# Kernel tuning notes

Hardware: AMD Instinct MI355X
Metric: run time of the kernel (lower is better)

Reference implementation:

```python
import jax, jax.numpy as jnp
import numpy as np

D_MODEL = 128; D_STATE = 64; HEADDIM = 32; D_CONV = 4; EXPAND = 2
D_INNER = EXPAND * D_MODEL          # 256
NHEADS = D_INNER // HEADDIM         # 8
NGROUPS = 1
D_CONV_CH = D_INNER + 2 * NGROUPS * D_STATE      # 384
D_IN_PROJ = 2 * D_INNER + 2 * NGROUPS * D_STATE + NHEADS  # 648


def _mamba2(u, Win, convw, convb, dtb, Alog, Dp, normw, Wout):
    # u: (B, L, d_model). Mamba2 forward (ngroups=1, rmsnorm gated, no in/out bias).
    B, L, _ = u.shape
    zxbcdt = u @ Win                                   # (B,L,648)
    z, xBC, dt = jnp.split(zxbcdt, [D_INNER, D_INNER + D_CONV_CH], axis=-1)
    # depthwise causal conv1d (kernel D_CONV) + SiLU
    xp = jnp.pad(xBC, ((0, 0), (D_CONV - 1, 0), (0, 0)))
    xconv = sum(xp[:, k:k + L, :] * convw[k] for k in range(D_CONV)) + convb
    xBC = jax.nn.silu(xconv)
    x, Bm, Cm = jnp.split(xBC, [D_INNER, D_INNER + NGROUPS * D_STATE], axis=-1)
    dt = jax.nn.softplus(dt + dtb)                     # (B,L,H)
    A = -jnp.exp(Alog)                                 # (H,)
    xh = x.reshape(B, L, NHEADS, HEADDIM)              # (B,L,H,P)
    dA = jnp.exp(dt * A)                               # (B,L,H)

    def step(h, inp):
        dA_t, dt_t, B_t, C_t, x_t = inp
        h = h * dA_t[:, :, None, None] + jnp.einsum('bh,bn,bhp->bhpn', dt_t, B_t, x_t)
        y = jnp.einsum('bhpn,bn->bhp', h, C_t)
        return h, y

    h0 = jnp.zeros((B, NHEADS, HEADDIM, D_STATE), dtype=u.dtype)
    xs = (jnp.moveaxis(dA, 1, 0), jnp.moveaxis(dt, 1, 0), jnp.moveaxis(Bm, 1, 0),
          jnp.moveaxis(Cm, 1, 0), jnp.moveaxis(xh, 1, 0))
    _, ys = jax.lax.scan(step, h0, xs)
    y = jnp.moveaxis(ys, 0, 1) + Dp[None, None, :, None] * xh   # skip D
    y = y.reshape(B, L, D_INNER)
    # RMSNormGated (norm_before_gate=False): rmsnorm(y * silu(z)) * weight
    y = y * jax.nn.silu(z)
    y = y * jax.lax.rsqrt(jnp.mean(y * y, axis=-1, keepdims=True) + 1e-5) * normw
    return y @ Wout


def _cross_attn(x, ctx, Wq, bq, Wk, bk, Wv, bv, Wo, bo):
    Q = x @ Wq + bq
    K = ctx @ Wk + bk
    V = ctx @ Wv + bv
    att = jax.nn.softmax(jnp.einsum('bqd,bkd->bqk', Q, K) * (D_MODEL ** -0.5), axis=-1)
    return jnp.einsum('bqk,bkd->bqd', att, V) @ Wo + bo


def setup_inputs() -> dict:
    key = jax.random.key(0)
    ks = jax.random.split(key, 8)
    B, L = 2048, 8

    def lin(k, fi, fo):
        return jax.random.normal(k, (fi, fo), jnp.float32) / np.sqrt(fi)

    def mamba_params(kseq):
        k = jax.random.split(kseq, 6)
        dt = jax.random.uniform(k[3], (NHEADS,), minval=0.001, maxval=0.1)
        return {
            'Win': lin(k[0], D_MODEL, D_IN_PROJ),
            'convw': jax.random.normal(k[1], (D_CONV, D_CONV_CH), jnp.float32) * 0.2,
            'convb': jnp.zeros((D_CONV_CH,), jnp.float32),
            'dtb': dt + jnp.log(-jnp.expm1(-dt)),  # inverse softplus
            'Alog': jnp.log(jax.random.uniform(k[4], (NHEADS,), minval=1.0, maxval=16.0)),
            'D': jnp.ones((NHEADS,), jnp.float32),
            'normw': jnp.ones((D_INNER,), jnp.float32),
            'Wout': lin(k[5], D_INNER, D_MODEL),
        }

    inp = {
        'st_feature': jax.random.normal(ks[0], (B, L, D_MODEL), jnp.float32),
        'exp_feature': jax.random.normal(ks[1], (B, L, D_MODEL), jnp.float32),
    }
    for pref, p in (('st_', mamba_params(ks[2])), ('ex_', mamba_params(ks[3]))):
        for n, v in p.items():
            inp[pref + n] = v

    def ca(kseq, pref):
        k = jax.random.split(kseq, 4)
        d = {}
        for n, kk in zip(('Wq', 'Wk', 'Wv', 'Wo'), k):
            d[pref + n] = lin(kk, D_MODEL, D_MODEL)
            d[pref + 'b' + n[1]] = jnp.zeros((D_MODEL,), jnp.float32)
        return d

    inp.update(ca(ks[4], 'cx_'))  # cross_atten_exp
    inp.update(ca(ks[5], 'cs_'))  # cross_atten_st
    inp['mlp_W'] = lin(ks[6], 8 * 2 * D_MODEL, 1024)
    inp['mlp_b'] = jnp.zeros((1024,), jnp.float32)
    return inp


def reference(st_feature, exp_feature,
              st_Win, st_convw, st_convb, st_dtb, st_Alog, st_D, st_normw, st_Wout,
              ex_Win, ex_convw, ex_convb, ex_dtb, ex_Alog, ex_D, ex_normw, ex_Wout,
              cx_Wq, cx_bq, cx_Wk, cx_bk, cx_Wv, cx_bv, cx_Wo, cx_bo,
              cs_Wq, cs_bq, cs_Wk, cs_bk, cs_Wv, cs_bv, cs_Wo, cs_bo,
              mlp_W, mlp_b):
    exp_f = _mamba2(exp_feature, ex_Win, ex_convw, ex_convb, ex_dtb, ex_Alog, ex_D, ex_normw, ex_Wout)
    st_f = _mamba2(st_feature, st_Win, st_convw, st_convb, st_dtb, st_Alog, st_D, st_normw, st_Wout)
    exp_a = _cross_attn(exp_f, st_f, cx_Wq, cx_bq, cx_Wk, cx_bk, cx_Wv, cx_bv, cx_Wo, cx_bo)
    st_a = _cross_attn(st_f, exp_f, cs_Wq, cs_bq, cs_Wk, cs_bk, cs_Wv, cs_bv, cs_Wo, cs_bo)
    x = jnp.concatenate([st_a, exp_a], axis=-1)        # (B, 8, 256)
    x = x.reshape(x.shape[0], -1)                      # (B, 2048)
    return x @ mlp_W + mlp_b
```

## Files before the change

kernel.cpp:

```cpp
#include <hip/hip_runtime.h>
#include <hip/hip_bf16.h>
#include <math.h>

#define B_SZ 2048
#define L_SEQ 8
#define DMODEL 128
#define DSTATE 64
#define HEADDIM 32
#define DCONV 4
#define DINNER 256
#define NHEADS 8
#define DCONVCH 384
#define DINPROJ 648
#define NPAD 656

typedef short bf16x8 __attribute__((ext_vector_type(8)));
typedef float floatx4 __attribute__((ext_vector_type(4)));

__device__ __forceinline__ float siluf(float x) {
    return x / (1.f + expf(-x));
}
__device__ __forceinline__ float bf2f(unsigned short h) {
    unsigned int u = ((unsigned int)h) << 16;
    return __builtin_bit_cast(float, u);
}
__device__ __forceinline__ unsigned short f2bf(float f) {
    __hip_bfloat16 b = __float2bfloat16(f);
    return __builtin_bit_cast(unsigned short, b);
}
__device__ __forceinline__ void unpack8(bf16x8 v, float* o) {
    #pragma unroll
    for (int j = 0; j < 8; ++j) o[j] = bf2f((unsigned short)v[j]);
}

__global__ __launch_bounds__(256) void prep_weights(
    const float* __restrict__ st_Win, const float* __restrict__ ex_Win,
    const float* __restrict__ st_Wout, const float* __restrict__ ex_Wout,
    const float* __restrict__ cs_Wq, const float* __restrict__ cs_Wk,
    const float* __restrict__ cs_Wv, const float* __restrict__ cs_Wo,
    const float* __restrict__ cx_Wq, const float* __restrict__ cx_Wk,
    const float* __restrict__ cx_Wv, const float* __restrict__ cx_Wo,
    unsigned short* __restrict__ winT_st, unsigned short* __restrict__ winT_ex,
    unsigned short* __restrict__ woutT_st, unsigned short* __restrict__ woutT_ex,
    unsigned short* __restrict__ attnWT)
{
    int blk = blockIdx.x;
    if (blk < 656) {
        const float* src = blk < 328 ? st_Win : ex_Win;
        unsigned short* dst = blk < 328 ? winT_st : winT_ex;
        int idx = (blk % 328) * 256 + threadIdx.x;
        if (idx >= NPAD * 128) return;
        int n = idx / 128, k = idx % 128;
        float v = (n < DINPROJ) ? src[k * DINPROJ + n] : 0.f;
        dst[idx] = f2bf(v);
    } else if (blk < 912) {
        const float* src = blk < 784 ? st_Wout : ex_Wout;
        unsigned short* dst = blk < 784 ? woutT_st : woutT_ex;
        int idx = ((blk - 656) % 128) * 256 + threadIdx.x;
        int n = idx / 256, k = idx % 256;
        dst[idx] = f2bf(src[k * 128 + n]);
    } else {
        int b2 = blk - 912;
        int mat = b2 >> 6;
        const float* src = mat == 0 ? cs_Wq : mat == 1 ? cs_Wk : mat == 2 ? cs_Wv :
                           mat == 3 ? cs_Wo : mat == 4 ? cx_Wq : mat == 5 ? cx_Wk :
                           mat == 6 ? cx_Wv : cx_Wo;
        int e = (b2 & 63) * 256 + threadIdx.x;
        int n = e >> 7, k = e & 127;
        attnWT[mat * 16384 + n * 128 + k] = f2bf(src[k * 128 + n]);
    }
}

#define LDK 136
#define LDZ 648
#define LDY 264
__global__ __launch_bounds__(256, 4) void mamba_dual(
    const float* __restrict__ u_ex, const float* __restrict__ u_st,
    const unsigned short* __restrict__ WinT_ex, const unsigned short* __restrict__ WinT_st,
    const float* __restrict__ convw_ex, const float* __restrict__ convw_st,
    const float* __restrict__ convb_ex, const float* __restrict__ convb_st,
    const float* __restrict__ dtb_ex, const float* __restrict__ dtb_st,
    const float* __restrict__ Alog_ex, const float* __restrict__ Alog_st,
    const float* __restrict__ Dp_ex, const float* __restrict__ Dp_st,
    const float* __restrict__ normw_ex, const float* __restrict__ normw_st,
    const unsigned short* __restrict__ WoutT_ex, const unsigned short* __restrict__ WoutT_st,
    unsigned short* __restrict__ out_ex, unsigned short* __restrict__ out_st)
{
    const int which = blockIdx.x >> 10;
    const float* u = which ? u_st : u_ex;
    const unsigned short* WinT = which ? WinT_st : WinT_ex;
    const float* convw = which ? convw_st : convw_ex;
    const float* convb = which ? convb_st : convb_ex;
    const float* dtb = which ? dtb_st : dtb_ex;
    const float* Alog = which ? Alog_st : Alog_ex;
    const float* Dp = which ? Dp_st : Dp_ex;
    const float* normw = which ? normw_st : normw_ex;
    const unsigned short* WoutT = which ? WoutT_st : WoutT_ex;
    unsigned short* outf = which ? out_st : out_ex;

    const int tid = threadIdx.x;
    const int lane = tid & 63;
    const int wave = tid >> 6;
    const int l15 = lane & 15;
    const int q8 = (lane >> 4) * 8;
    const int row0 = (lane >> 4) * 4;
    const int grow0 = (blockIdx.x & 1023) * 16;

    __shared__ __align__(16) unsigned short uA[16 * LDK];
    __shared__ __align__(16) unsigned short zx[16 * LDZ];
    __shared__ __align__(16) unsigned short yb[16 * LDY];
    __shared__ float dtraw[16][8];
    __shared__ float dtv[2][8][8];
    __shared__ float cum[2][8][8];
    __shared__ float Gm[2][8][8];
    __shared__ float red[16][32];
    __shared__ float rstd[16];
    float* coefp = (float*)uA;

    for (int i = tid; i < 512; i += 256) {
        int r = i >> 5, k4 = (i & 31) * 4;
        float4 v = *(const float4*)(u + (size_t)(grow0 + r) * DMODEL + k4);
        ushort4 h;
        h.x = f2bf(v.x); h.y = f2bf(v.y); h.z = f2bf(v.z); h.w = f2bf(v.w);
        *(ushort4*)(uA + r * LDK + k4) = h;
    }
    __syncthreads();

    {
        bf16x8 af[4];
        #pragma unroll
        for (int kk = 0; kk < 4; ++kk)
            af[kk] = *(const bf16x8*)(uA + l15 * LDK + kk * 32 + q8);
        for (int nt = wave; nt < 41; nt += 4) {
            floatx4 acc = {0.f, 0.f, 0.f, 0.f};
            const unsigned short* bp = WinT + (size_t)(nt * 16 + l15) * 128 + q8;
            #pragma unroll
            for (int kk = 0; kk < 4; ++kk) {
                bf16x8 bf = *(const bf16x8*)(bp + kk * 32);
                acc = __builtin_amdgcn_mfma_f32_16x16x32_bf16(af[kk], bf, acc, 0, 0, 0);
            }
            if (nt == 40) {
                if (l15 < 8) {
                    #pragma unroll
                    for (int r = 0; r < 4; ++r)
                        dtraw[row0 + r][l15] = acc[r];
                }
            } else {
                #pragma unroll
                for (int r = 0; r < 4; ++r)
                    zx[(row0 + r) * LDZ + nt * 16 + l15] = f2bf(acc[r]);
            }
        }
    }
    __syncthreads();

    float cv[3][8];
    {
        #pragma unroll
        for (int it = 0; it < 3; ++it) {
            int i = tid + it * 256;
            int r = i / 48, g = i % 48;
            int c0 = g * 8;
            int l = r & 7, bloc = r >> 3;
            float s[8];
            float4 cb0 = *(const float4*)(convb + c0);
            float4 cb1 = *(const float4*)(convb + c0 + 4);
            s[0] = cb0.x; s[1] = cb0.y; s[2] = cb0.z; s[3] = cb0.w;
            s[4] = cb1.x; s[5] = cb1.y; s[6] = cb1.z; s[7] = cb1.w;
            #pragma unroll
            for (int k = 0; k < DCONV; ++k) {
                int lp = l + k - (DCONV - 1);
                if (lp >= 0) {
                    bf16x8 v = *(const bf16x8*)(zx + (bloc * 8 + lp) * LDZ + 256 + c0);
                    float vf[8];
                    unpack8(v, vf);
                    float4 w0 = *(const float4*)(convw + k * DCONVCH + c0);
                    float4 w1 = *(const float4*)(convw + k * DCONVCH + c0 + 4);
                    s[0] += vf[0] * w0.x; s[1] += vf[1] * w0.y;
                    s[2] += vf[2] * w0.z; s[3] += vf[3] * w0.w;
                    s[4] += vf[4] * w1.x; s[5] += vf[5] * w1.y;
                    s[6] += vf[6] * w1.z; s[7] += vf[7] * w1.w;
                }
            }
            #pragma unroll
            for (int j = 0; j < 8; ++j) cv[it][j] = siluf(s[j]);
        }
        if (tid < 128) {
            int r = tid >> 3, h = tid & 7;
            float v = dtraw[r][h] + dtb[h];
            dtv[r >> 3][r & 7][h] = (v > 20.f) ? v : log1pf(expf(v));
        }
    }
    __syncthreads();
    {
        #pragma unroll
        for (int it = 0; it < 3; ++it) {
            int i = tid + it * 256;
            int r = i / 48, c0 = (i % 48) * 8;
            bf16x8 o;
            #pragma unroll
            for (int j = 0; j < 8; ++j) o[j] = (short)f2bf(cv[it][j]);
            *(bf16x8*)(zx + r * LDZ + 256 + c0) = o;
        }
    }
    __syncthreads();

    if (tid < 128) {
        int bloc = tid >> 6, t = (tid >> 3) & 7, s = tid & 7;
        float a = 0.f;
        #pragma unroll
        for (int n = 0; n < DSTATE; n += 8) {
            bf16x8 bv = *(const bf16x8*)(zx + (bloc * 8 + s) * LDZ + 512 + n);
            bf16x8 cvv = *(const bf16x8*)(zx + (bloc * 8 + t) * LDZ + 576 + n);
            float bf_[8], cf_[8];
            unpack8(bv, bf_); unpack8(cvv, cf_);
            #pragma unroll
            for (int j = 0; j < 8; ++j) a += bf_[j] * cf_[j];
        }
        Gm[bloc][t][s] = a;
    } else if (tid < 144) {
        int j = tid - 128;
        int bloc = j >> 3, h = j & 7;
        float c = 0.f;
        for (int l = 0; l < L_SEQ; ++l) { c += dtv[bloc][l][h]; cum[bloc][l][h] = c; }
    }
    __syncthreads();

    for (int i = tid; i < 1024; i += 256) {
        int bloc = i >> 9, t = (i >> 6) & 7, s = (i >> 3) & 7, h = i & 7;
        float A = -expf(Alog[h]);
        coefp[i] = (s <= t)
            ? Gm[bloc][t][s] * expf(A * (cum[bloc][t][h] - cum[bloc][s][h])) * dtv[bloc][s][h]
            : 0.f;
    }
    __syncthreads();

    {
        #pragma unroll
        for (int it = 0; it < 2; ++it) {
            int i = tid + it * 256;
            int r = i >> 5, g = i & 31;
            int c0 = g * 8, h = g >> 2;
            int bloc = r >> 3, t = r & 7;
            float acc[8];
            {
                bf16x8 xv = *(const bf16x8*)(zx + r * LDZ + 256 + c0);
                float xf[8]; unpack8(xv, xf);
                float d = Dp[h];
                #pragma unroll
                for (int j = 0; j < 8; ++j) acc[j] = d * xf[j];
            }
            for (int s = 0; s <= t; ++s) {
                float cf = coefp[((bloc * 8 + t) * 8 + s) * 8 + h];
                bf16x8 xv = *(const bf16x8*)(zx + (bloc * 8 + s) * LDZ + 256 + c0);
                float xf[8]; unpack8(xv, xf);
                #pragma unroll
                for (int j = 0; j < 8; ++j) acc[j] += cf * xf[j];
            }
            bf16x8 zv = *(const bf16x8*)(zx + r * LDZ + c0);
            float zf[8]; unpack8(zv, zf);
            float p = 0.f;
            bf16x8 o;
            #pragma unroll
            for (int j = 0; j < 8; ++j) {
                float y = acc[j] * siluf(zf[j]);
                p += y * y;
                o[j] = (short)f2bf(y);
            }
            *(bf16x8*)(yb + r * LDY + c0) = o;
            red[r][g] = p;
        }
    }
    __syncthreads();
    if (tid < 16) {
        float s = 0.f;
        #pragma unroll
        for (int j = 0; j < 32; ++j) s += red[tid][j];
        rstd[tid] = rsqrtf(s / (float)DINNER + 1e-5f);
    }
    __syncthreads();
    {
        #pragma unroll
        for (int it = 0; it < 2; ++it) {
            int i = tid + it * 256;
            int r = i >> 5, c0 = (i & 31) * 8;
            bf16x8 v = *(const bf16x8*)(yb + r * LDY + c0);
            float vf[8]; unpack8(v, vf);
            float4 w0 = *(const float4*)(normw + c0);
            float4 w1 = *(const float4*)(normw + c0 + 4);
            float rs = rstd[r];
            bf16x8 o;
            o[0] = (short)f2bf(vf[0] * rs * w0.x); o[1] = (short)f2bf(vf[1] * rs * w0.y);
            o[2] = (short)f2bf(vf[2] * rs * w0.z); o[3] = (short)f2bf(vf[3] * rs * w0.w);
            o[4] = (short)f2bf(vf[4] * rs * w1.x); o[5] = (short)f2bf(vf[5] * rs * w1.y);
            o[6] = (short)f2bf(vf[6] * rs * w1.z); o[7] = (short)f2bf(vf[7] * rs * w1.w);
            *(bf16x8*)(yb + r * LDY + c0) = o;
        }
    }
    __syncthreads();

    {
        bf16x8 af[8];
        #pragma unroll
        for (int kk = 0; kk < 8; ++kk)
            af[kk] = *(const bf16x8*)(yb + l15 * LDY + kk * 32 + q8);
        #pragma unroll
        for (int ni = 0; ni < 2; ++ni) {
            int nt = wave * 2 + ni;
            floatx4 acc = {0.f, 0.f, 0.f, 0.f};
            const unsigned short* bp = WoutT + (size_t)(nt * 16 + l15) * 256 + q8;
            #pragma unroll
            for (int kk = 0; kk < 8; ++kk) {
                bf16x8 bf = *(const bf16x8*)(bp + kk * 32);
                acc = __builtin_amdgcn_mfma_f32_16x16x32_bf16(af[kk], bf, acc, 0, 0, 0);
            }
            #pragma unroll
            for (int r = 0; r < 4; ++r)
                outf[(size_t)(grow0 + row0 + r) * DMODEL + nt * 16 + l15] = f2bf(acc[r]);
        }
    }
}

#define ASTR 136
#define VSTR 40
#define PSTR 40
__global__ __launch_bounds__(256) void attn_kernel(
    const unsigned short* __restrict__ st_f,
    const unsigned short* __restrict__ exp_f,
    const unsigned short* __restrict__ WT,
    const float* __restrict__ cs_bq, const float* __restrict__ cs_bk,
    const float* __restrict__ cs_bv, const float* __restrict__ cs_bo,
    const float* __restrict__ cx_bq, const float* __restrict__ cx_bk,
    const float* __restrict__ cx_bv, const float* __restrict__ cx_bo,
    __hip_bfloat16* __restrict__ x)
{
    const int tid = threadIdx.x;
    const int lane = tid & 63, wave = tid >> 6;
    const int l15 = lane & 15;
    const int q8 = (lane >> 4) * 8;
    const int row0 = (lane >> 4) * 4;
    const int grow0 = blockIdx.x * 16;
    const int b0 = blockIdx.x * 2;
    const float scale = 0.08838834764831845f;

    __shared__ __align__(16) unsigned short stf[16 * ASTR];
    __shared__ __align__(16) unsigned short exf[16 * ASTR];
    __shared__ __align__(16) unsigned short Qs[16 * ASTR];
    __shared__ __align__(16) unsigned short Ks[16 * ASTR];
    __shared__ __align__(16) unsigned short Vt[128 * VSTR];
    __shared__ __align__(16) unsigned short P[16 * PSTR];
    __shared__ __align__(16) unsigned short attv[16 * ASTR];
    __shared__ float Ss[16][17];

    {
        int r = tid >> 4, c8 = (tid & 15) * 8;
        *(uint4*)(stf + r * ASTR + c8) = *(const uint4*)(st_f + (size_t)(grow0 + r) * 128 + c8);
        *(uint4*)(exf + r * ASTR + c8) = *(const uint4*)(exp_f + (size_t)(grow0 + r) * 128 + c8);
    }
    {
        int r = tid >> 1, c = 16 + (tid & 1) * 8;
        uint4 z = {0u, 0u, 0u, 0u};
        *(uint4*)(Vt + r * VSTR + c) = z;
    }
    __syncthreads();

    #pragma unroll
    for (int pass = 0; pass < 2; ++pass) {
        const unsigned short* qsrc = pass ? exf : stf;
        const unsigned short* kvsrc = pass ? stf : exf;
        const unsigned short* Wq = WT + (size_t)pass * 4 * 16384;
        const unsigned short* Wk = Wq + 16384;
        const unsigned short* Wv = Wq + 32768;
        const unsigned short* Wo = Wq + 49152;
        const float* bq = pass ? cx_bq : cs_bq;
        const float* bk = pass ? cx_bk : cs_bk;
        const float* bv = pass ? cx_bv : cs_bv;
        const float* bo = pass ? cx_bo : cs_bo;

        bf16x8 aq[4], akv[4];
        #pragma unroll
        for (int kk = 0; kk < 4; ++kk) {
            aq[kk]  = *(const bf16x8*)(qsrc  + l15 * ASTR + kk * 32 + q8);
            akv[kk] = *(const bf16x8*)(kvsrc + l15 * ASTR + kk * 32 + q8);
        }
        #pragma unroll
        for (int ni = 0; ni < 2; ++ni) {
            int nt = wave * 2 + ni;
            int nc = nt * 16 + l15;
            floatx4 accq = {0.f, 0.f, 0.f, 0.f};
            floatx4 acck = {0.f, 0.f, 0.f, 0.f};
            floatx4 accv = {0.f, 0.f, 0.f, 0.f};
            #pragma unroll
            for (int kk = 0; kk < 4; ++kk) {
                bf16x8 wqf = *(const bf16x8*)(Wq + (size_t)nc * 128 + kk * 32 + q8);
                bf16x8 wkf = *(const bf16x8*)(Wk + (size_t)nc * 128 + kk * 32 + q8);
                bf16x8 wvf = *(const bf16x8*)(Wv + (size_t)nc * 128 + kk * 32 + q8);
                accq = __builtin_amdgcn_mfma_f32_16x16x32_bf16(aq[kk],  wqf, accq, 0, 0, 0);
                acck = __builtin_amdgcn_mfma_f32_16x16x32_bf16(akv[kk], wkf, acck, 0, 0, 0);
                accv = __builtin_amdgcn_mfma_f32_16x16x32_bf16(akv[kk], wvf, accv, 0, 0, 0);
            }
            float bqv = bq[nc], bkv = bk[nc], bvv = bv[nc];
            #pragma unroll
            for (int r = 0; r < 4; ++r) {
                Qs[(row0 + r) * ASTR + nc] = f2bf(accq[r] + bqv);
                Ks[(row0 + r) * ASTR + nc] = f2bf(acck[r] + bkv);
                Vt[nc * VSTR + row0 + r]   = f2bf(accv[r] + bvv);
            }
        }
        __syncthreads();

        if (wave == 0) {
            floatx4 s = {0.f, 0.f, 0.f, 0.f};
            #pragma unroll
            for (int kk = 0; kk < 4; ++kk) {
                bf16x8 a = *(const bf16x8*)(Qs + l15 * ASTR + kk * 32 + q8);
                bf16x8 b = *(const bf16x8*)(Ks + l15 * ASTR + kk * 32 + q8);
                s = __builtin_amdgcn_mfma_f32_16x16x32_bf16(a, b, s, 0, 0, 0);
            }
            #pragma unroll
            for (int r = 0; r < 4; ++r) Ss[row0 + r][l15] = s[r];
        }
        __syncthreads();

        if (tid < 16) {
            int r = tid, c0 = (r >> 3) * 8;
            float v[8], mx = -1e30f;
            #pragma unroll
            for (int c = 0; c < 8; ++c) {
                v[c] = Ss[r][c0 + c] * scale;
                mx = fmaxf(mx, v[c]);
            }
            float sum = 0.f;
            #pragma unroll
            for (int c = 0; c < 8; ++c) { v[c] = expf(v[c] - mx); sum += v[c]; }
            float inv = 1.f / sum;
            #pragma unroll
            for (int c = 0; c < 32; ++c) {
                float pv = (c >= c0 && c < c0 + 8) ? v[c - c0] * inv : 0.f;
                P[r * PSTR + c] = f2bf(pv);
            }
        }
        __syncthreads();

        {
            bf16x8 ap = *(const bf16x8*)(P + l15 * PSTR + q8);
            #pragma unroll
            for (int ni = 0; ni < 2; ++ni) {
                int nc = (wave * 2 + ni) * 16 + l15;
                bf16x8 bv_ = *(const bf16x8*)(Vt + nc * VSTR + q8);
                floatx4 o = {0.f, 0.f, 0.f, 0.f};
                o = __builtin_amdgcn_mfma_f32_16x16x32_bf16(ap, bv_, o, 0, 0, 0);
                #pragma unroll
                for (int r = 0; r < 4; ++r)
                    attv[(row0 + r) * ASTR + nc] = f2bf(o[r]);
            }
        }
        __syncthreads();

        {
            bf16x8 ao[4];
            #pragma unroll
            for (int kk = 0; kk < 4; ++kk)
                ao[kk] = *(const bf16x8*)(attv + l15 * ASTR + kk * 32 + q8);
            #pragma unroll
            for (int ni = 0; ni < 2; ++ni) {
                int nc = (wave * 2 + ni) * 16 + l15;
                floatx4 acc = {0.f, 0.f, 0.f, 0.f};
                #pragma unroll
                for (int kk = 0; kk < 4; ++kk) {
                    bf16x8 wof = *(const bf16x8*)(Wo + (size_t)nc * 128 + kk * 32 + q8);
                    acc = __builtin_amdgcn_mfma_f32_16x16x32_bf16(ao[kk], wof, acc, 0, 0, 0);
                }
                float bov = bo[nc];
                #pragma unroll
                for (int r = 0; r < 4; ++r) {
                    int rr = row0 + r;
                    int bb = b0 + (rr >> 3), q = rr & 7;
                    x[(size_t)bb * 2048 + q * 256 + pass * 128 + nc] =
                        __float2bfloat16(acc[r] + bov);
                }
            }
        }
        __syncthreads();
    }
}

__global__ __launch_bounds__(256) void transpose_w_bf16(
    const float* __restrict__ W, unsigned short* __restrict__ Wt)
{
    __shared__ float tile[32][33];
    const int k0 = blockIdx.y * 32;
    const int n0 = blockIdx.x * 32;
    const int tid = threadIdx.x;
    const int c = tid & 31, r0 = tid >> 5;
    for (int rr = r0; rr < 32; rr += 8)
        tile[rr][c] = W[(k0 + rr) * 1024 + n0 + c];
    __syncthreads();
    for (int rr = r0; rr < 32; rr += 8)
        Wt[(size_t)(n0 + rr) * 2048 + k0 + c] = f2bf(tile[c][rr]);
}

#define LDT 40
__global__ __launch_bounds__(256) void mlp_mfma(
    const unsigned short* __restrict__ X,
    const unsigned short* __restrict__ Wt,
    const float* __restrict__ bias,
    float* __restrict__ out)
{
    __shared__ __align__(16) unsigned short As[64 * LDT];
    __shared__ __align__(16) unsigned short Bs[64 * LDT];
    const int tid = threadIdx.x;
    const int wave = tid >> 6, lane = tid & 63;
    const int wm = (wave >> 1) * 32, wn = (wave & 1) * 32;
    const int bm = blockIdx.y * 64, bn = blockIdx.x * 64;

    const int lrow = tid >> 2;
    const int lcol = (tid & 3) * 8;
    const int l15 = lane & 15;
    const int q8 = (lane >> 4) * 8;

    floatx4 acc00 = {0.f, 0.f, 0.f, 0.f};
    floatx4 acc01 = {0.f, 0.f, 0.f, 0.f};
    floatx4 acc10 = {0.f, 0.f, 0.f, 0.f};
    floatx4 acc11 = {0.f, 0.f, 0.f, 0.f};

    const unsigned short* gA = X + (size_t)(bm + lrow) * 2048 + lcol;
    const unsigned short* gB = Wt + (size_t)(bn + lrow) * 2048 + lcol;

    for (int k0 = 0; k0 < 2048; k0 += 32) {
        uint4 av = *(const uint4*)(gA + k0);
        uint4 bv = *(const uint4*)(gB + k0);
        __syncthreads();
        *(uint4*)(As + lrow * LDT + lcol) = av;
        *(uint4*)(Bs + lrow * LDT + lcol) = bv;
        __syncthreads();
        bf16x8 a0 = *(const bf16x8*)(As + (wm + l15) * LDT + q8);
        bf16x8 a1 = *(const bf16x8*)(As + (wm + 16 + l15) * LDT + q8);
        bf16x8 b0 = *(const bf16x8*)(Bs + (wn + l15) * LDT + q8);
        bf16x8 b1 = *(const bf16x8*)(Bs + (wn + 16 + l15) * LDT + q8);
        acc00 = __builtin_amdgcn_mfma_f32_16x16x32_bf16(a0, b0, acc00, 0, 0, 0);
        acc01 = __builtin_amdgcn_mfma_f32_16x16x32_bf16(a0, b1, acc01, 0, 0, 0);
        acc10 = __builtin_amdgcn_mfma_f32_16x16x32_bf16(a1, b0, acc10, 0, 0, 0);
        acc11 = __builtin_amdgcn_mfma_f32_16x16x32_bf16(a1, b1, acc11, 0, 0, 0);
    }

    const int row0 = (lane >> 4) * 4;
    #pragma unroll
    for (int j = 0; j < 2; ++j) {
        int col = bn + wn + j * 16 + l15;
        float bv = bias[col];
        floatx4 aj0 = j ? acc01 : acc00;
        floatx4 aj1 = j ? acc11 : acc10;
        #pragma unroll
        for (int r = 0; r < 4; ++r) {
            out[(size_t)(bm + wm + row0 + r) * 1024 + col] = aj0[r] + bv;
            out[(size_t)(bm + wm + 16 + row0 + r) * 1024 + col] = aj1[r] + bv;
        }
    }
}

extern "C" void kernel_launch(void* const* d_in, const int* in_sizes, int n_in,
                              void* d_out, int out_size, void* d_ws, size_t ws_size,
                              hipStream_t stream) {
    const float* st_feature = (const float*)d_in[0];
    const float* exp_feature = (const float*)d_in[1];
    const float* st_Win = (const float*)d_in[2];
    const float* st_convw = (const float*)d_in[3];
    const float* st_convb = (const float*)d_in[4];
    const float* st_dtb = (const float*)d_in[5];
    const float* st_Alog = (const float*)d_in[6];
    const float* st_D = (const float*)d_in[7];
    const float* st_normw = (const float*)d_in[8];
    const float* st_Wout = (const float*)d_in[9];
    const float* ex_Win = (const float*)d_in[10];
    const float* ex_convw = (const float*)d_in[11];
    const float* ex_convb = (const float*)d_in[12];
    const float* ex_dtb = (const float*)d_in[13];
    const float* ex_Alog = (const float*)d_in[14];
    const float* ex_D = (const float*)d_in[15];
    const float* ex_normw = (const float*)d_in[16];
    const float* ex_Wout = (const float*)d_in[17];
    const float* cx_Wq = (const float*)d_in[18]; const float* cx_bq = (const float*)d_in[19];
    const float* cx_Wk = (const float*)d_in[20]; const float* cx_bk = (const float*)d_in[21];
    const float* cx_Wv = (const float*)d_in[22]; const float* cx_bv = (const float*)d_in[23];
    const float* cx_Wo = (const float*)d_in[24]; const float* cx_bo = (const float*)d_in[25];
    const float* cs_Wq = (const float*)d_in[26]; const float* cs_bq = (const float*)d_in[27];
    const float* cs_Wk = (const float*)d_in[28]; const float* cs_bk = (const float*)d_in[29];
    const float* cs_Wv = (const float*)d_in[30]; const float* cs_bv = (const float*)d_in[31];
    const float* cs_Wo = (const float*)d_in[32]; const float* cs_bo = (const float*)d_in[33];
    const float* mlp_W = (const float*)d_in[34];
    const float* mlp_b = (const float*)d_in[35];

    unsigned short* wsu = (unsigned short*)d_ws;
    unsigned short* st_fb  = wsu;
    unsigned short* exp_fb = st_fb + (size_t)B_SZ * L_SEQ * DMODEL;
    unsigned short* xbuf   = exp_fb + (size_t)B_SZ * L_SEQ * DMODEL;
    unsigned short* wtbuf  = xbuf + (size_t)2048 * 2048;
    unsigned short* winT_st = wtbuf + (size_t)1024 * 2048;
    unsigned short* winT_ex = winT_st + (size_t)NPAD * 128;
    unsigned short* woutT_st = winT_ex + (size_t)NPAD * 128;
    unsigned short* woutT_ex = woutT_st + (size_t)128 * 256;
    unsigned short* attnWT  = woutT_ex + (size_t)128 * 256;

    prep_weights<<<1424, 256, 0, stream>>>(
        st_Win, ex_Win, st_Wout, ex_Wout,
        cs_Wq, cs_Wk, cs_Wv, cs_Wo, cx_Wq, cx_Wk, cx_Wv, cx_Wo,
        winT_st, winT_ex, woutT_st, woutT_ex, attnWT);
    {
        dim3 g(1024 / 32, 2048 / 32);
        transpose_w_bf16<<<g, 256, 0, stream>>>(mlp_W, wtbuf);
    }
    mamba_dual<<<2048, 256, 0, stream>>>(
        exp_feature, st_feature, winT_ex, winT_st,
        ex_convw, st_convw, ex_convb, st_convb,
        ex_dtb, st_dtb, ex_Alog, st_Alog, ex_D, st_D,
        ex_normw, st_normw, woutT_ex, woutT_st,
        exp_fb, st_fb);
    attn_kernel<<<B_SZ / 2, 256, 0, stream>>>(st_fb, exp_fb, attnWT,
                                              cs_bq, cs_bk, cs_bv, cs_bo,
                                              cx_bq, cx_bk, cx_bv, cx_bo,
                                              (__hip_bfloat16*)xbuf);
    {
        dim3 g(1024 / 64, 2048 / 64);
        mlp_mfma<<<g, 256, 0, stream>>>(xbuf, wtbuf, mlp_b, (float*)d_out);
    }
}
```

Baseline: 273.7 us.

## Merge MLP weight transpose into prep, double attention tile, use direct-to-LDS loads in MLP

The MLP weight transpose now runs as extra blocks of the prep_weights launch, which removes one kernel launch. The attention kernel handles 32 rows (4 batches) per block instead of 16, so each projection weight fragment feeds two MFMAs and all four waves share the score computation. The MLP GEMM uses a K-step of 64, XOR-swizzled LDS tiles and global_load_lds direct-to-LDS copies in place of register staging. The cost is more LDS per block and fewer blocks, which can lower occupancy and parallelism in the attention kernel.

```diff
diff --git a/kernel.cpp b/kernel.cpp
--- a/kernel.cpp
+++ b/kernel.cpp
@@ -32,6 +32,11 @@
     #pragma unroll
     for (int j = 0; j < 8; ++j) o[j] = bf2f((unsigned short)v[j]);
 }
+__device__ __forceinline__ void gl_lds16(const unsigned short* g, unsigned short* l) {
+    __builtin_amdgcn_global_load_lds(
+        (const __attribute__((address_space(1))) unsigned int*)g,
+        (__attribute__((address_space(3))) unsigned int*)l, 16, 0, 0);
+}
 
 __global__ __launch_bounds__(256) void prep_weights(
     const float* __restrict__ st_Win, const float* __restrict__ ex_Win,
@@ -40,10 +45,12 @@
     const float* __restrict__ cs_Wv, const float* __restrict__ cs_Wo,
     const float* __restrict__ cx_Wq, const float* __restrict__ cx_Wk,
     const float* __restrict__ cx_Wv, const float* __restrict__ cx_Wo,
+    const float* __restrict__ mlp_W,
     unsigned short* __restrict__ winT_st, unsigned short* __restrict__ winT_ex,
     unsigned short* __restrict__ woutT_st, unsigned short* __restrict__ woutT_ex,
-    unsigned short* __restrict__ attnWT)
+    unsigned short* __restrict__ attnWT, unsigned short* __restrict__ mlpWt)
 {
+    __shared__ float tile[32][33];
     int blk = blockIdx.x;
     if (blk < 656) {
         const float* src = blk < 328 ? st_Win : ex_Win;
@@ -59,7 +66,7 @@
         int idx = ((blk - 656) % 128) * 256 + threadIdx.x;
         int n = idx / 256, k = idx % 256;
         dst[idx] = f2bf(src[k * 128 + n]);
-    } else {
+    } else if (blk < 1424) {
         int b2 = blk - 912;
         int mat = b2 >> 6;
         const float* src = mat == 0 ? cs_Wq : mat == 1 ? cs_Wk : mat == 2 ? cs_Wv :
@@ -68,6 +75,16 @@
         int e = (b2 & 63) * 256 + threadIdx.x;
         int n = e >> 7, k = e & 127;
         attnWT[mat * 16384 + n * 128 + k] = f2bf(src[k * 128 + n]);
+    } else {
+        int b2 = blk - 1424;
+        int n0 = (b2 & 31) * 32, k0 = (b2 >> 5) * 32;
+        const int tid = threadIdx.x;
+        const int c = tid & 31, r0 = tid >> 5;
+        for (int rr = r0; rr < 32; rr += 8)
+            tile[rr][c] = mlp_W[(size_t)(k0 + rr) * 1024 + n0 + c];
+        __syncthreads();
+        for (int rr = r0; rr < 32; rr += 8)
+            mlpWt[(size_t)(n0 + rr) * 2048 + k0 + c] = f2bf(tile[c][rr]);
     }
 }
 
@@ -324,7 +341,7 @@
 #define ASTR 136
 #define VSTR 40
 #define PSTR 40
-__global__ __launch_bounds__(256) void attn_kernel(
+__global__ __launch_bounds__(256, 2) void attn_kernel(
     const unsigned short* __restrict__ st_f,
     const unsigned short* __restrict__ exp_f,
     const unsigned short* __restrict__ WT,
@@ -339,28 +356,25 @@
     const int l15 = lane & 15;
     const int q8 = (lane >> 4) * 8;
     const int row0 = (lane >> 4) * 4;
-    const int grow0 = blockIdx.x * 16;
-    const int b0 = blockIdx.x * 2;
+    const int grow0 = blockIdx.x * 32;
+    const int b0 = blockIdx.x * 4;
     const float scale = 0.08838834764831845f;
 
-    __shared__ __align__(16) unsigned short stf[16 * ASTR];
-    __shared__ __align__(16) unsigned short exf[16 * ASTR];
-    __shared__ __align__(16) unsigned short Qs[16 * ASTR];
-    __shared__ __align__(16) unsigned short Ks[16 * ASTR];
+    __shared__ __align__(16) unsigned short stf[32 * ASTR];
+    __shared__ __align__(16) unsigned short exf[32 * ASTR];
+    __shared__ __align__(16) unsigned short Qs[32 * ASTR];
+    __shared__ __align__(16) unsigned short Ks[32 * ASTR];
+    __shared__ __align__(16) unsigned short attv[32 * ASTR];
     __shared__ __align__(16) unsigned short Vt[128 * VSTR];
-    __shared__ __align__(16) unsigned short P[16 * PSTR];
-    __shared__ __align__(16) unsigned short attv[16 * ASTR];
-    __shared__ float Ss[16][17];
-
-    {
-        int r = tid >> 4, c8 = (tid & 15) * 8;
+    __shared__ __align__(16) unsigned short P[32 * PSTR];
+    __shared__ float Ss[32][33];
+
+    #pragma unroll
+    for (int it = 0; it < 2; ++it) {
+        int i = tid + it * 256;
+        int r = i >> 4, c8 = (i & 15) * 8;
         *(uint4*)(stf + r * ASTR + c8) = *(const uint4*)(st_f + (size_t)(grow0 + r) * 128 + c8);
         *(uint4*)(exf + r * ASTR + c8) = *(const uint4*)(exp_f + (size_t)(grow0 + r) * 128 + c8);
-    }
-    {
-        int r = tid >> 1, c = 16 + (tid & 1) * 8;
-        uint4 z = {0u, 0u, 0u, 0u};
-        *(uint4*)(Vt + r * VSTR + c) = z;
     }
     __syncthreads();
 
@@ -377,52 +391,63 @@
         const float* bv = pass ? cx_bv : cs_bv;
         const float* bo = pass ? cx_bo : cs_bo;
 
-        bf16x8 aq[4], akv[4];
-        #pragma unroll
-        for (int kk = 0; kk < 4; ++kk) {
-            aq[kk]  = *(const bf16x8*)(qsrc  + l15 * ASTR + kk * 32 + q8);
-            akv[kk] = *(const bf16x8*)(kvsrc + l15 * ASTR + kk * 32 + q8);
-        }
-        #pragma unroll
-        for (int ni = 0; ni < 2; ++ni) {
-            int nt = wave * 2 + ni;
-            int nc = nt * 16 + l15;
-            floatx4 accq = {0.f, 0.f, 0.f, 0.f};
-            floatx4 acck = {0.f, 0.f, 0.f, 0.f};
-            floatx4 accv = {0.f, 0.f, 0.f, 0.f};
+        {
+            bf16x8 aq[2][4], akv[2][4];
+            #pragma unroll
+            for (int mt = 0; mt < 2; ++mt)
+                #pragma unroll
+                for (int kk = 0; kk < 4; ++kk) {
+                    aq[mt][kk]  = *(const bf16x8*)(qsrc  + (mt * 16 + l15) * ASTR + kk * 32 + q8);
+                    akv[mt][kk] = *(const bf16x8*)(kvsrc + (mt * 16 + l15) * ASTR + kk * 32 + q8);
+                }
+            #pragma unroll
+            for (int ni = 0; ni < 2; ++ni) {
+                int nc = (wave * 2 + ni) * 16 + l15;
+                floatx4 aq0 = {0,0,0,0}, aq1 = {0,0,0,0};
+                floatx4 ak0 = {0,0,0,0}, ak1 = {0,0,0,0};
+                floatx4 av0 = {0,0,0,0}, av1 = {0,0,0,0};
+                #pragma unroll
+                for (int kk = 0; kk < 4; ++kk) {
+                    bf16x8 wqf = *(const bf16x8*)(Wq + (size_t)nc * 128 + kk * 32 + q8);
+                    bf16x8 wkf = *(const bf16x8*)(Wk + (size_t)nc * 128 + kk * 32 + q8);
+                    bf16x8 wvf = *(const bf16x8*)(Wv + (size_t)nc * 128 + kk * 32 + q8);
+                    aq0 = __builtin_amdgcn_mfma_f32_16x16x32_bf16(aq[0][kk],  wqf, aq0, 0, 0, 0);
+                    aq1 = __builtin_amdgcn_mfma_f32_16x16x32_bf16(aq[1][kk],  wqf, aq1, 0, 0, 0);
+                    ak0 = __builtin_amdgcn_mfma_f32_16x16x32_bf16(akv[0][kk], wkf, ak0, 0, 0, 0);
+                    ak1 = __builtin_amdgcn_mfma_f32_16x16x32_bf16(akv[1][kk], wkf, ak1, 0, 0, 0);
+                    av0 = __builtin_amdgcn_mfma_f32_16x16x32_bf16(akv[0][kk], wvf, av0, 0, 0, 0);
+                    av1 = __builtin_amdgcn_mfma_f32_16x16x32_bf16(akv[1][kk], wvf, av1, 0, 0, 0);
+                }
+                float bqv = bq[nc], bkv = bk[nc], bvv = bv[nc];
+                #pragma unroll
+                for (int r = 0; r < 4; ++r) {
+                    Qs[(row0 + r) * ASTR + nc]      = f2bf(aq0[r] + bqv);
+                    Qs[(16 + row0 + r) * ASTR + nc] = f2bf(aq1[r] + bqv);
+                    Ks[(row0 + r) * ASTR + nc]      = f2bf(ak0[r] + bkv);
+                    Ks[(16 + row0 + r) * ASTR + nc] = f2bf(ak1[r] + bkv);
+                    Vt[nc * VSTR + row0 + r]        = f2bf(av0[r] + bvv);
+                    Vt[nc * VSTR + 16 + row0 + r]   = f2bf(av1[r] + bvv);
+                }
+            }
+        }
+        __syncthreads();
+
+        {
+            int mtS = wave >> 1, ntS = wave & 1;
+            floatx4 s = {0,0,0,0};
             #pragma unroll
             for (int kk = 0; kk < 4; ++kk) {
-                bf16x8 wqf = *(const bf16x8*)(Wq + (size_t)nc * 128 + kk * 32 + q8);
-                bf16x8 wkf = *(const bf16x8*)(Wk + (size_t)nc * 128 + kk * 32 + q8);
-                bf16x8 wvf = *(const bf16x8*)(Wv + (size_t)nc * 128 + kk * 32 + q8);
-                accq = __builtin_amdgcn_mfma_f32_16x16x32_bf16(aq[kk],  wqf, accq, 0, 0, 0);
-                acck = __builtin_amdgcn_mfma_f32_16x16x32_bf16(akv[kk], wkf, acck, 0, 0, 0);
-                accv = __builtin_amdgcn_mfma_f32_16x16x32_bf16(akv[kk], wvf, accv, 0, 0, 0);
-            }
-            float bqv = bq[nc], bkv = bk[nc], bvv = bv[nc];
-            #pragma unroll
-            for (int r = 0; r < 4; ++r) {
-                Qs[(row0 + r) * ASTR + nc] = f2bf(accq[r] + bqv);
-                Ks[(row0 + r) * ASTR + nc] = f2bf(acck[r] + bkv);
-                Vt[nc * VSTR + row0 + r]   = f2bf(accv[r] + bvv);
-            }
-        }
-        __syncthreads();
-
-        if (wave == 0) {
-            floatx4 s = {0.f, 0.f, 0.f, 0.f};
-            #pragma unroll
-            for (int kk = 0; kk < 4; ++kk) {
-                bf16x8 a = *(const bf16x8*)(Qs + l15 * ASTR + kk * 32 + q8);
-                bf16x8 b = *(const bf16x8*)(Ks + l15 * ASTR + kk * 32 + q8);
+                bf16x8 a = *(const bf16x8*)(Qs + (mtS * 16 + l15) * ASTR + kk * 32 + q8);
+                bf16x8 b = *(const bf16x8*)(Ks + (ntS * 16 + l15) * ASTR + kk * 32 + q8);
                 s = __builtin_amdgcn_mfma_f32_16x16x32_bf16(a, b, s, 0, 0, 0);
             }
             #pragma unroll
-            for (int r = 0; r < 4; ++r) Ss[row0 + r][l15] = s[r];
-        }
-        __syncthreads();
-
-        if (tid < 16) {
+            for (int r = 0; r < 4; ++r)
+                Ss[mtS * 16 + row0 + r][ntS * 16 + l15] = s[r];
+        }
+        __syncthreads();
+
+        if (tid < 32) {
             int r = tid, c0 = (r >> 3) * 8;
             float v[8], mx = -1e30f;
             #pragma unroll
@@ -443,105 +468,110 @@
         __syncthreads();
 
         {
-            bf16x8 ap = *(const bf16x8*)(P + l15 * PSTR + q8);
             #pragma unroll
             for (int ni = 0; ni < 2; ++ni) {
                 int nc = (wave * 2 + ni) * 16 + l15;
                 bf16x8 bv_ = *(const bf16x8*)(Vt + nc * VSTR + q8);
-                floatx4 o = {0.f, 0.f, 0.f, 0.f};
-                o = __builtin_amdgcn_mfma_f32_16x16x32_bf16(ap, bv_, o, 0, 0, 0);
-                #pragma unroll
-                for (int r = 0; r < 4; ++r)
-                    attv[(row0 + r) * ASTR + nc] = f2bf(o[r]);
+                #pragma unroll
+                for (int mt = 0; mt < 2; ++mt) {
+                    bf16x8 ap = *(const bf16x8*)(P + (mt * 16 + l15) * PSTR + q8);
+                    floatx4 o = {0,0,0,0};
+                    o = __builtin_amdgcn_mfma_f32_16x16x32_bf16(ap, bv_, o, 0, 0, 0);
+                    #pragma unroll
+                    for (int r = 0; r < 4; ++r)
+                        attv[(mt * 16 + row0 + r) * ASTR + nc] = f2bf(o[r]);
+                }
             }
         }
         __syncthreads();
 
         {
-            bf16x8 ao[4];
-            #pragma unroll
-            for (int kk = 0; kk < 4; ++kk)
-                ao[kk] = *(const bf16x8*)(attv + l15 * ASTR + kk * 32 + q8);
+            bf16x8 ao[2][4];
+            #pragma unroll
+            for (int mt = 0; mt < 2; ++mt)
+                #pragma unroll
+                for (int kk = 0; kk < 4; ++kk)
+                    ao[mt][kk] = *(const bf16x8*)(attv + (mt * 16 + l15) * ASTR + kk * 32 + q8);
             #pragma unroll
             for (int ni = 0; ni < 2; ++ni) {
                 int nc = (wave * 2 + ni) * 16 + l15;
-                floatx4 acc = {0.f, 0.f, 0.f, 0.f};
+                floatx4 a0 = {0,0,0,0}, a1 = {0,0,0,0};
                 #pragma unroll
                 for (int kk = 0; kk < 4; ++kk) {
                     bf16x8 wof = *(const bf16x8*)(Wo + (size_t)nc * 128 + kk * 32 + q8);
-                    acc = __builtin_amdgcn_mfma_f32_16x16x32_bf16(ao[kk], wof, acc, 0, 0, 0);
+                    a0 = __builtin_amdgcn_mfma_f32_16x16x32_bf16(ao[0][kk], wof, a0, 0, 0, 0);
+                    a1 = __builtin_amdgcn_mfma_f32_16x16x32_bf16(ao[1][kk], wof, a1, 0, 0, 0);
                 }
                 float bov = bo[nc];
                 #pragma unroll
                 for (int r = 0; r < 4; ++r) {
-                    int rr = row0 + r;
-                    int bb = b0 + (rr >> 3), q = rr & 7;
-                    x[(size_t)bb * 2048 + q * 256 + pass * 128 + nc] =
-                        __float2bfloat16(acc[r] + bov);
-                }
-            }
-        }
-        __syncthreads();
-    }
-}
-
-__global__ __launch_bounds__(256) void transpose_w_bf16(
-    const float* __restrict__ W, unsigned short* __restrict__ Wt)
-{
-    __shared__ float tile[32][33];
-    const int k0 = blockIdx.y * 32;
-    const int n0 = blockIdx.x * 32;
-    const int tid = threadIdx.x;
-    const int c = tid & 31, r0 = tid >> 5;
-    for (int rr = r0; rr < 32; rr += 8)
-        tile[rr][c] = W[(k0 + rr) * 1024 + n0 + c];
-    __syncthreads();
-    for (int rr = r0; rr < 32; rr += 8)
-        Wt[(size_t)(n0 + rr) * 2048 + k0 + c] = f2bf(tile[c][rr]);
-}
-
-#define LDT 40
-__global__ __launch_bounds__(256) void mlp_mfma(
+                    int rr0 = row0 + r;
+                    int rr1 = 16 + row0 + r;
+                    x[(size_t)(b0 + (rr0 >> 3)) * 2048 + (rr0 & 7) * 256 + pass * 128 + nc] =
+                        __float2bfloat16(a0[r] + bov);
+                    x[(size_t)(b0 + (rr1 >> 3)) * 2048 + (rr1 & 7) * 256 + pass * 128 + nc] =
+                        __float2bfloat16(a1[r] + bov);
+                }
+            }
+        }
+        __syncthreads();
+    }
+}
+
+__global__ __launch_bounds__(256, 2) void mlp_mfma(
     const unsigned short* __restrict__ X,
     const unsigned short* __restrict__ Wt,
     const float* __restrict__ bias,
     float* __restrict__ out)
 {
-    __shared__ __align__(16) unsigned short As[64 * LDT];
-    __shared__ __align__(16) unsigned short Bs[64 * LDT];
+    __shared__ __align__(16) unsigned short As[64 * 64];
+    __shared__ __align__(16) unsigned short Bs[64 * 64];
     const int tid = threadIdx.x;
     const int wave = tid >> 6, lane = tid & 63;
     const int wm = (wave >> 1) * 32, wn = (wave & 1) * 32;
     const int bm = blockIdx.y * 64, bn = blockIdx.x * 64;
-
-    const int lrow = tid >> 2;
-    const int lcol = (tid & 3) * 8;
-    const int l15 = lane & 15;
-    const int q8 = (lane >> 4) * 8;
-
-    floatx4 acc00 = {0.f, 0.f, 0.f, 0.f};
-    floatx4 acc01 = {0.f, 0.f, 0.f, 0.f};
-    floatx4 acc10 = {0.f, 0.f, 0.f, 0.f};
-    floatx4 acc11 = {0.f, 0.f, 0.f, 0.f};
-
-    const unsigned short* gA = X + (size_t)(bm + lrow) * 2048 + lcol;
-    const unsigned short* gB = Wt + (size_t)(bn + lrow) * 2048 + lcol;
-
-    for (int k0 = 0; k0 < 2048; k0 += 32) {
-        uint4 av = *(const uint4*)(gA + k0);
-        uint4 bv = *(const uint4*)(gB + k0);
-        __syncthreads();
-        *(uint4*)(As + lrow * LDT + lcol) = av;
-        *(uint4*)(Bs + lrow * LDT + lcol) = bv;
-        __syncthreads();
-        bf16x8 a0 = *(const bf16x8*)(As + (wm + l15) * LDT + q8);
-        bf16x8 a1 = *(const bf16x8*)(As + (wm + 16 + l15) * LDT + q8);
-        bf16x8 b0 = *(const bf16x8*)(Bs + (wn + l15) * LDT + q8);
-        bf16x8 b1 = *(const bf16x8*)(Bs + (wn + 16 + l15) * LDT + q8);
-        acc00 = __builtin_amdgcn_mfma_f32_16x16x32_bf16(a0, b0, acc00, 0, 0, 0);
-        acc01 = __builtin_amdgcn_mfma_f32_16x16x32_bf16(a0, b1, acc01, 0, 0, 0);
-        acc10 = __builtin_amdgcn_mfma_f32_16x16x32_bf16(a1, b0, acc10, 0, 0, 0);
-        acc11 = __builtin_amdgcn_mfma_f32_16x16x32_bf16(a1, b1, acc11, 0, 0, 0);
+    const int l15 = lane & 15, q8 = (lane >> 4) * 8;
+
+    const int c0i = tid, c1i = tid + 256;
+    const int r0s = c0i >> 3, c0s = ((c0i & 7) ^ (r0s & 7)) * 8;
+    const int r1s = c1i >> 3, c1s = ((c1i & 7) ^ (r1s & 7)) * 8;
+    const unsigned short* gA0 = X + (size_t)(bm + r0s) * 2048 + c0s;
+    const unsigned short* gA1 = X + (size_t)(bm + r1s) * 2048 + c1s;
+    const unsigned short* gB0 = Wt + (size_t)(bn + r0s) * 2048 + c0s;
+    const unsigned short* gB1 = Wt + (size_t)(bn + r1s) * 2048 + c1s;
+    unsigned short* lA0 = As + c0i * 8;
+    unsigned short* lA1 = As + c1i * 8;
+    unsigned short* lB0 = Bs + c0i * 8;
+    unsigned short* lB1 = Bs + c1i * 8;
+
+    floatx4 acc[2][2];
+    #pragma unroll
+    for (int i = 0; i < 2; ++i)
+        #pragma unroll
+        for (int j = 0; j < 2; ++j) acc[i][j] = (floatx4){0.f, 0.f, 0.f, 0.f};
+
+    const int ra0 = wm + l15, ra1 = wm + 16 + l15;
+    const int rb0 = wn + l15, rb1 = wn + 16 + l15;
+
+    for (int k0 = 0; k0 < 2048; k0 += 64) {
+        __syncthreads();
+        gl_lds16(gA0 + k0, lA0);
+        gl_lds16(gA1 + k0, lA1);
+        gl_lds16(gB0 + k0, lB0);
+        gl_lds16(gB1 + k0, lB1);
+        __syncthreads();
+        #pragma unroll
+        for (int ks = 0; ks < 2; ++ks) {
+            int xx = ks * 4 + (q8 >> 3);
+            bf16x8 a0 = *(const bf16x8*)(As + (ra0 * 8 + (xx ^ (ra0 & 7))) * 8);
+            bf16x8 a1 = *(const bf16x8*)(As + (ra1 * 8 + (xx ^ (ra1 & 7))) * 8);
+            bf16x8 b0 = *(const bf16x8*)(Bs + (rb0 * 8 + (xx ^ (rb0 & 7))) * 8);
+            bf16x8 b1 = *(const bf16x8*)(Bs + (rb1 * 8 + (xx ^ (rb1 & 7))) * 8);
+            acc[0][0] = __builtin_amdgcn_mfma_f32_16x16x32_bf16(a0, b0, acc[0][0], 0, 0, 0);
+            acc[0][1] = __builtin_amdgcn_mfma_f32_16x16x32_bf16(a0, b1, acc[0][1], 0, 0, 0);
+            acc[1][0] = __builtin_amdgcn_mfma_f32_16x16x32_bf16(a1, b0, acc[1][0], 0, 0, 0);
+            acc[1][1] = __builtin_amdgcn_mfma_f32_16x16x32_bf16(a1, b1, acc[1][1], 0, 0, 0);
+        }
     }
 
     const int row0 = (lane >> 4) * 4;
@@ -549,12 +579,10 @@
     for (int j = 0; j < 2; ++j) {
         int col = bn + wn + j * 16 + l15;
         float bv = bias[col];
-        floatx4 aj0 = j ? acc01 : acc00;
-        floatx4 aj1 = j ? acc11 : acc10;
         #pragma unroll
         for (int r = 0; r < 4; ++r) {
-            out[(size_t)(bm + wm + row0 + r) * 1024 + col] = aj0[r] + bv;
-            out[(size_t)(bm + wm + 16 + row0 + r) * 1024 + col] = aj1[r] + bv;
+            out[(size_t)(bm + wm + row0 + r) * 1024 + col] = acc[0][j][r] + bv;
+            out[(size_t)(bm + wm + 16 + row0 + r) * 1024 + col] = acc[1][j][r] + bv;
         }
     }
 }
@@ -602,21 +630,17 @@
     unsigned short* woutT_ex = woutT_st + (size_t)128 * 256;
     unsigned short* attnWT  = woutT_ex + (size_t)128 * 256;
 
-    prep_weights<<<1424, 256, 0, stream>>>(
+    prep_weights<<<3472, 256, 0, stream>>>(
         st_Win, ex_Win, st_Wout, ex_Wout,
-        cs_Wq, cs_Wk, cs_Wv, cs_Wo, cx_Wq, cx_Wk, cx_Wv, cx_Wo,
-        winT_st, winT_ex, woutT_st, woutT_ex, attnWT);
-    {
-        dim3 g(1024 / 32, 2048 / 32);
-        transpose_w_bf16<<<g, 256, 0, stream>>>(mlp_W, wtbuf);
-    }
+        cs_Wq, cs_Wk, cs_Wv, cs_Wo, cx_Wq, cx_Wk, cx_Wv, cx_Wo, mlp_W,
+        winT_st, winT_ex, woutT_st, woutT_ex, attnWT, wtbuf);
     mamba_dual<<<2048, 256, 0, stream>>>(
         exp_feature, st_feature, winT_ex, winT_st,
         ex_convw, st_convw, ex_convb, st_convb,
         ex_dtb, st_dtb, ex_Alog, st_Alog, ex_D, st_D,
         ex_normw, st_normw, woutT_ex, woutT_st,
         exp_fb, st_fb);
-    attn_kernel<<<B_SZ / 2, 256, 0, stream>>>(st_fb, exp_fb, attnWT,
+    attn_kernel<<<B_SZ / 4, 256, 0, stream>>>(st_fb, exp_fb, attnWT,
                                               cs_bq, cs_bk, cs_bv, cs_bo,
                                               cx_bq, cx_bk, cx_bv, cx_bo,
                                               (__hip_bfloat16*)xbuf);
```

New measurement: 253.5 us. 1.08x faster.
